# Optimization experiments

Measured on AMD Instinct MI355X. Metric: run time of the kernel, lower is better.

## Reference

```python
import jax, jax.numpy as jnp
import numpy as np

N_NODES = 50000
N_EDGES = 300000
N_ETYPES = 4
D = 256          # input_dim == output_dim (no zero-pad branch in GatedGraphConv)
RES = 768        # res_feature_dim
N_GRAPHS = 128
N_STEPS = 8
HID = 256        # classifier hidden dim


def setup_inputs() -> dict:
    key = jax.random.key(0)
    ks = jax.random.split(key, 12)
    s = 0.05
    return {
        "features": jax.random.normal(ks[0], (N_NODES, D + RES), jnp.float32),
        "W_e": jax.random.normal(ks[1], (N_ETYPES, D, D), jnp.float32) * s,
        "b_e": jnp.zeros((N_ETYPES, D), jnp.float32),
        "W_ih": jax.random.normal(ks[2], (D, 3 * D), jnp.float32) * s,
        "W_hh": jax.random.normal(ks[3], (D, 3 * D), jnp.float32) * s,
        "b_ih": jnp.zeros((3 * D,), jnp.float32),
        "b_hh": jnp.zeros((3 * D,), jnp.float32),
        "W1": jax.random.normal(ks[4], (D + RES, HID), jnp.float32) * s,
        "b1": jnp.zeros((HID,), jnp.float32),
        "W2": jax.random.normal(ks[5], (HID, 1), jnp.float32) * s,
        "b2": jnp.zeros((1,), jnp.float32),
        "src": jax.random.randint(ks[6], (N_EDGES,), 0, N_NODES),
        "dst": jax.random.randint(ks[7], (N_EDGES,), 0, N_NODES),
        "etypes": jax.random.randint(ks[8], (N_EDGES,), 0, N_ETYPES),
        "node2graph": jnp.sort(jax.random.randint(ks[9], (N_NODES,), 0, N_GRAPHS)),
    }


def _gru_cell(x, h, W_ih, W_hh, b_ih, b_hh):
    # PyTorch GRUCell, gate order (r, z, n)
    gi = x @ W_ih + b_ih
    gh = h @ W_hh + b_hh
    i_r, i_z, i_n = jnp.split(gi, 3, axis=-1)
    h_r, h_z, h_n = jnp.split(gh, 3, axis=-1)
    r = jax.nn.sigmoid(i_r + h_r)
    z = jax.nn.sigmoid(i_z + h_z)
    n = jnp.tanh(i_n + r * h_n)
    return (1.0 - z) * n + z * h


def reference(features, W_e, b_e, W_ih, W_hh, b_ih, b_hh, W1, b1, W2, b2,
              src, dst, etypes, node2graph):
    h = features[:, :D]          # node features fed to GGNN
    res = features[:, D:]        # mixed residual features (bypass GGNN)

    def step(h, _):
        # per-edge-type linear on all nodes: [T, N, D]
        ht = jnp.einsum('nd,tde->tne', h, W_e) + b_e[:, None, :]
        msgs = ht[etypes, src]                                   # [E, D]
        a = jax.ops.segment_sum(msgs, dst, num_segments=N_NODES)  # scatter-add to dst
        return _gru_cell(a, h, W_ih, W_hh, b_ih, b_hh), None

    h, _ = jax.lax.scan(step, h, None, length=N_STEPS)

    out = jnp.concatenate([h, res], axis=1)  # [N, D+RES]
    # masked mean over nodes of each graph == segment mean
    sums = jax.ops.segment_sum(out, node2graph, num_segments=N_GRAPHS)
    cnts = jax.ops.segment_sum(jnp.ones((N_NODES,), out.dtype), node2graph,
                               num_segments=N_GRAPHS)
    pooled = sums / jnp.maximum(cnts, 1.0)[:, None]  # [B, D+RES]

    # classifier (dropouts inactive at eval): Linear -> ReLU -> Linear -> sigmoid
    hcls = jax.nn.relu(pooled @ W1 + b1)
    logits = hcls @ W2 + b2
    return jax.nn.sigmoid(logits)  # [B, 1]
```

## Files before the change

### kernel.cpp

```cpp
#include <hip/hip_runtime.h>
#include <math.h>
#include <stdint.h>

#define NN 50000
#define NE 300000
#define NT4 200000
#define NG 128
#define NSTEP 8
#define MPAD 50048
#define SCB 196
#define SCB2 782
#define PCH 8
#define EM 64
#define ECAP 896

typedef __attribute__((ext_vector_type(8))) short bf16x8;
typedef __attribute__((ext_vector_type(8))) unsigned short u16x8;
typedef __attribute__((ext_vector_type(4))) float f32x4;
typedef unsigned short u16;
typedef unsigned int u32;

__device__ __forceinline__ float b2f(u16 u) {
  union { u32 i; float f; } c; c.i = ((u32)u) << 16; return c.f;
}
__device__ __forceinline__ u16 f2b(float f) {
  union { float f; u32 i; } c; c.f = f;
  u32 x = c.i;
  u32 r = (x + 0x7fffu + ((x >> 16) & 1u)) >> 16;
  return (u16)r;
}

__device__ __forceinline__ void load_lds16(const void* g, void* l) {
  __builtin_amdgcn_global_load_lds((const __attribute__((address_space(1))) u32*)g,
                                   (__attribute__((address_space(3))) u32*)l, 16, 0, 0);
}

__global__ void k_conv_we(const float* __restrict__ W_e, u16* __restrict__ Wt) {
  int i = blockIdx.x * 256 + threadIdx.x;
  int c = i >> 8, d = i & 255;
  Wt[c * 256 + d] = f2b(W_e[(c >> 8) * 65536 + d * 256 + (c & 255)]);
}
__global__ void k_conv_rz(const float* __restrict__ W_ih, const float* __restrict__ W_hh,
                          u16* __restrict__ ah, u16* __restrict__ ha) {
  int i = blockIdx.x * 256 + threadIdx.x;
  int n = i >> 9, k = i & 511;
  float va = (k < 256) ? W_ih[k * 768 + n] : W_hh[(k - 256) * 768 + n];
  float vh = (k < 256) ? W_hh[k * 768 + n] : W_ih[(k - 256) * 768 + n];
  ah[n * 512 + k] = f2b(va);
  ha[n * 512 + k] = f2b(vh);
}
__global__ void k_conv_n(const float* __restrict__ W, u16* __restrict__ Wt) {
  int i = blockIdx.x * 256 + threadIdx.x;
  int n = i >> 8, k = i & 255;
  Wt[n * 256 + k] = f2b(W[k * 768 + 512 + n]);
}
__global__ void k_brz(const float* __restrict__ b_ih, const float* __restrict__ b_hh,
                      float* __restrict__ b_rz) {
  int i = blockIdx.x * 256 + threadIdx.x;
  if (i < 512) b_rz[i] = b_ih[i] + b_hh[i];
}

__global__ void k_init_h(const float* __restrict__ feat, u16* __restrict__ acat) {
  int i = blockIdx.x * 256 + threadIdx.x;
  int n = i >> 6, d = (i & 63) << 2;
  ushort4 o;
  if (n < NN) {
    float4 v = *(const float4*)(feat + (size_t)n * 1024 + d);
    o.x = f2b(v.x); o.y = f2b(v.y); o.z = f2b(v.z); o.w = f2b(v.w);
  } else {
    o.x = o.y = o.z = o.w = 0;
  }
  *(ushort4*)(acat + (size_t)n * 768 + d) = o;
}

__global__ void k_hist(const int* __restrict__ dst, const int* __restrict__ ety,
                       int* __restrict__ deg2) {
  int e = blockIdx.x * 256 + threadIdx.x;
  if (e < NE) atomicAdd(&deg2[dst[e] * 4 + ety[e]], 1);
}
__global__ void k_scan1(const int* __restrict__ deg2, int* __restrict__ part, int* __restrict__ bsum) {
  __shared__ int sh[256];
  int b = blockIdx.x, t = threadIdx.x;
  int i = b * 256 + t;
  int v = (i < NT4) ? deg2[i] : 0;
  sh[t] = v;
  __syncthreads();
  for (int off = 1; off < 256; off <<= 1) {
    int tmp = (t >= off) ? sh[t - off] : 0;
    __syncthreads();
    sh[t] += tmp;
    __syncthreads();
  }
  if (i < NT4) part[i] = sh[t] - v;
  if (t == 255) bsum[b] = sh[255];
}
__global__ void k_scan2(const int* __restrict__ bsum, int* __restrict__ boff) {
  __shared__ int sh[1024];
  int t = threadIdx.x;
  int v = (t < SCB2) ? bsum[t] : 0;
  sh[t] = v;
  __syncthreads();
  for (int off = 1; off < 1024; off <<= 1) {
    int tmp = (t >= off) ? sh[t - off] : 0;
    __syncthreads();
    sh[t] += tmp;
    __syncthreads();
  }
  boff[t] = sh[t] - v;
  if (t == 1023) boff[1024] = sh[1023];
}
__global__ void k_scan3(const int* __restrict__ part, const int* __restrict__ boff, int* __restrict__ rp2) {
  int i = blockIdx.x * 256 + threadIdx.x;
  if (i < NT4) rp2[i] = part[i] + boff[i >> 8];
  if (i == NT4) rp2[NT4] = boff[1024];
}
__global__ void k_scatter(const int* __restrict__ src, const int* __restrict__ dst,
                          const int* __restrict__ ety, const int* __restrict__ rp2,
                          int* __restrict__ cursor2, int* __restrict__ esrc) {
  int e = blockIdx.x * 256 + threadIdx.x;
  if (e < NE) {
    int seg = dst[e] * 4 + ety[e];
    int p = rp2[seg] + atomicAdd(&cursor2[seg], 1);
    esrc[p] = src[e];
  }
}
__global__ void k_cnt2(const int* __restrict__ deg2, ushort4* __restrict__ cnt2) {
  int v = blockIdx.x * 256 + threadIdx.x;
  if (v >= MPAD) return;
  ushort4 o;
  if (v < NN) {
    o.x = (u16)deg2[v * 4 + 0]; o.y = (u16)deg2[v * 4 + 1];
    o.z = (u16)deg2[v * 4 + 2]; o.w = (u16)deg2[v * 4 + 3];
  } else {
    o.x = o.y = o.z = o.w = 0;
  }
  cnt2[v] = o;
}
__global__ void k_gstart(const int* __restrict__ n2g, int* __restrict__ gstart) {
  int n = blockIdx.x * 256 + threadIdx.x;
  if (n >= NN) return;
  int g = n2g[n];
  int gp = (n == 0) ? -1 : n2g[n - 1];
  for (int x = gp + 1; x <= g; ++x) gstart[x] = n;
  if (n == NN - 1)
    for (int x = g + 1; x <= NG; ++x) gstart[x] = NN;
}

__global__ __launch_bounds__(512, 4) void k_eagg(
    const u16* __restrict__ acat, int hboff,
    const int* __restrict__ rp2, const int* __restrict__ esrc,
    const u16* __restrict__ Wt_e, const u16* __restrict__ Wt_in,
    const ushort4* __restrict__ cnt2, const float* __restrict__ b_e,
    const float* __restrict__ b_ih512,
    u16* __restrict__ acat_out, u16* __restrict__ inb) {
  __shared__ __align__(16) char Ss[EM * 512];
  __shared__ __align__(16) char Bs[256 * 128];
  __shared__ int Es[ECAP];
  __shared__ int Rp[257];
  const int tid = threadIdx.x;
  const int wv = tid >> 6, l = tid & 63;
  const int hw = tid >> 5, lw = tid & 31;
  const int m0 = blockIdx.x * EM;
  const int fr = l & 15, kq = l >> 4;
  const int wm = (wv >> 2) * 32, wn = (wv & 3) * 64;

  const int base4 = m0 * 4;
  const int e0 = rp2[base4];
  for (int i = tid; i <= 256; i += 512) {
    int idx = base4 + i;
    if (idx > NT4) idx = NT4;
    Rp[i] = rp2[idx] - e0;
  }
  {
    int idxe = base4 + 256;
    if (idxe > NT4) idxe = NT4;
    int ecnt = rp2[idxe] - e0;
    int ecl = ecnt < ECAP ? ecnt : ECAP;
    for (int i = tid; i < ecl; i += 512) Es[i] = esrc[e0 + i] * 768 + hboff;
  }
  __syncthreads();

  f32x4 acc[2][4];
#pragma unroll
  for (int m = 0; m < 2; ++m)
#pragma unroll
    for (int n = 0; n < 4; ++n) acc[m][n] = (f32x4){0.f, 0.f, 0.f, 0.f};

  for (int t = 0; t < 4; ++t) {
    if (t > 0) __syncthreads();
    int cc[4], ee[4];
#pragma unroll
    for (int rr = 0; rr < 4; ++rr) {
      int li = (hw * 4 + rr) * 4 + t;
      cc[rr] = Rp[li];
      ee[rr] = Rp[li + 1];
    }
    float ar[4][8];
#pragma unroll
    for (int rr = 0; rr < 4; ++rr)
#pragma unroll
      for (int q = 0; q < 8; ++q) ar[rr][q] = 0.f;
    bool more = (cc[0] < ee[0]) | (cc[1] < ee[1]) | (cc[2] < ee[2]) | (cc[3] < ee[3]);
    while (more) {
      u16x8 v[4];
      bool p[4];
#pragma unroll
      for (int rr = 0; rr < 4; ++rr) {
        p[rr] = cc[rr] < ee[rr];
        if (p[rr]) {
          int rel = cc[rr];
          int off = (rel < ECAP) ? Es[rel] : (esrc[e0 + rel] * 768 + hboff);
          v[rr] = *(const u16x8*)(acat + (size_t)off + lw * 8);
        }
      }
#pragma unroll
      for (int rr = 0; rr < 4; ++rr) {
        if (p[rr]) {
#pragma unroll
          for (int q = 0; q < 8; ++q) ar[rr][q] += b2f(v[rr][q]);
          cc[rr]++;
        }
      }
      more = (cc[0] < ee[0]) | (cc[1] < ee[1]) | (cc[2] < ee[2]) | (cc[3] < ee[3]);
    }
#pragma unroll
    for (int rr = 0; rr < 4; ++rr) {
      int row = hw * 4 + rr;
      u16x8 o;
#pragma unroll
      for (int q = 0; q < 8; ++q) o[q] = f2b(ar[rr][q]);
      *(u16x8*)(Ss + row * 512 + ((lw * 16) ^ ((row & 7) << 4))) = o;
    }

    const u16* Bw = Wt_e + (size_t)t * 65536;
    for (int kc = 0; kc < 4; ++kc) {
      __syncthreads();
#pragma unroll
      for (int pph = 0; pph < 4; ++pph) {
        int brow = pph * 64 + (tid >> 3);
        int ks = kc * 64 + (((tid & 7) ^ (brow & 7)) << 3);
        load_lds16(Bw + (size_t)brow * 256 + ks, Bs + pph * 8192 + wv * 1024);
      }
      asm volatile("s_waitcnt vmcnt(0)" ::: "memory");
      __syncthreads();
#pragma unroll
      for (int kk = 0; kk < 64; kk += 32) {
        bf16x8 af[2], bfr[4];
        int kb = (kk + kq * 8) * 2;
        int ka = (kc * 64 + kk + kq * 8) * 2;
#pragma unroll
        for (int m = 0; m < 2; ++m) {
          int R = wm + m * 16 + fr;
          af[m] = *(const bf16x8*)(Ss + R * 512 + (ka ^ ((R & 7) << 4)));
        }
#pragma unroll
        for (int n = 0; n < 4; ++n) {
          int R = wn + n * 16 + fr;
          bfr[n] = *(const bf16x8*)(Bs + R * 128 + (kb ^ ((R & 7) << 4)));
        }
#pragma unroll
        for (int m = 0; m < 2; ++m)
#pragma unroll
          for (int n = 0; n < 4; ++n)
            acc[m][n] = __builtin_amdgcn_mfma_f32_16x16x32_bf16(af[m], bfr[n], acc[m][n], 0, 0, 0);
      }
    }
  }
  __syncthreads();

  float bev[4][4];
#pragma unroll
  for (int n = 0; n < 4; ++n)
#pragma unroll
    for (int t = 0; t < 4; ++t) bev[n][t] = b_e[t * 256 + wn + n * 16 + fr];
#pragma unroll
  for (int m = 0; m < 2; ++m) {
#pragma unroll
    for (int j = 0; j < 4; ++j) {
      int r = wm + m * 16 + kq * 4 + j;
      int v = m0 + r;
      ushort4 c4 = cnt2[v];
      float c0 = c4.x, c1 = c4.y, c2 = c4.z, c3 = c4.w;
#pragma unroll
      for (int n = 0; n < 4; ++n) {
        int col = wn + n * 16 + fr;
        float val = acc[m][n][j] + c0 * bev[n][0] + c1 * bev[n][1] + c2 * bev[n][2] + c3 * bev[n][3];
        u16 vb = f2b(val);
        acat_out[(size_t)v * 768 + 256 + col] = vb;
        *(u16*)(Ss + r * 512 + ((col * 2) ^ ((r & 7) << 4))) = vb;
      }
    }
  }
#pragma unroll
  for (int m = 0; m < 2; ++m)
#pragma unroll
    for (int n = 0; n < 4; ++n) acc[m][n] = (f32x4){0.f, 0.f, 0.f, 0.f};

  for (int kc = 0; kc < 4; ++kc) {
    __syncthreads();
#pragma unroll
    for (int pph = 0; pph < 4; ++pph) {
      int brow = pph * 64 + (tid >> 3);
      int ks = kc * 64 + (((tid & 7) ^ (brow & 7)) << 3);
      load_lds16(Wt_in + (size_t)brow * 256 + ks, Bs + pph * 8192 + wv * 1024);
    }
    asm volatile("s_waitcnt vmcnt(0)" ::: "memory");
    __syncthreads();
#pragma unroll
    for (int kk = 0; kk < 64; kk += 32) {
      bf16x8 af[2], bfr[4];
      int kb = (kk + kq * 8) * 2;
      int ka = (kc * 64 + kk + kq * 8) * 2;
#pragma unroll
      for (int m = 0; m < 2; ++m) {
        int R = wm + m * 16 + fr;
        af[m] = *(const bf16x8*)(Ss + R * 512 + (ka ^ ((R & 7) << 4)));
      }
#pragma unroll
      for (int n = 0; n < 4; ++n) {
        int R = wn + n * 16 + fr;
        bfr[n] = *(const bf16x8*)(Bs + R * 128 + (kb ^ ((R & 7) << 4)));
      }
#pragma unroll
      for (int m = 0; m < 2; ++m)
#pragma unroll
        for (int n = 0; n < 4; ++n)
          acc[m][n] = __builtin_amdgcn_mfma_f32_16x16x32_bf16(af[m], bfr[n], acc[m][n], 0, 0, 0);
    }
  }
  float bi[4];
#pragma unroll
  for (int n = 0; n < 4; ++n) bi[n] = b_ih512[wn + n * 16 + fr];
#pragma unroll
  for (int m = 0; m < 2; ++m) {
#pragma unroll
    for (int j = 0; j < 4; ++j) {
      int v = m0 + wm + m * 16 + kq * 4 + j;
#pragma unroll
      for (int n = 0; n < 4; ++n) {
        int col = wn + n * 16 + fr;
        inb[(size_t)v * 256 + col] = f2b(acc[m][n][j] + bi[n]);
      }
    }
  }
}

template <int MODE>
__global__ __launch_bounds__(512, 2) void k_gemm2(
    const u16* __restrict__ A, int lda, int K,
    const u16* __restrict__ Bt, const float* __restrict__ bias,
    u16* __restrict__ C, int ldc,
    const u16* __restrict__ rzb, const u16* __restrict__ inb,
    const u16* __restrict__ hold, u16* __restrict__ hnew) {
  __shared__ __align__(16) char AsB[2][64 * 128];
  __shared__ __align__(16) char BsB[2][256 * 128];
  const int tid = threadIdx.x;
  const int wv = tid >> 6, l = tid & 63;
  const int m0 = blockIdx.y * 64, n0 = blockIdx.x * 256;
  const int fr = l & 15, kq = l >> 4;
  const int wm = (wv >> 2) * 32, wn = (wv & 3) * 64;
  const int arow = tid >> 3, acl = tid & 7;

  f32x4 acc[2][4];
#pragma unroll
  for (int m = 0; m < 2; ++m)
#pragma unroll
    for (int n = 0; n < 4; ++n) acc[m][n] = (f32x4){0.f, 0.f, 0.f, 0.f};

  auto stage = [&](int buf, int k0) {
    load_lds16(A + (size_t)(m0 + arow) * lda + k0 + ((acl ^ (arow & 7)) << 3),
               AsB[buf] + wv * 1024);
#pragma unroll
    for (int p = 0; p < 4; ++p) {
      int brow = p * 64 + arow;
      load_lds16(Bt + (size_t)(n0 + brow) * K + k0 + ((acl ^ (brow & 7)) << 3),
                 BsB[buf] + p * 8192 + wv * 1024);
    }
  };

  stage(0, 0);
  const int NK = K >> 6;
  for (int ki = 0; ki < NK; ++ki) {
    const int cur = ki & 1;
    if (ki + 1 < NK) {
      stage(cur ^ 1, (ki + 1) << 6);
      asm volatile("s_waitcnt vmcnt(5)" ::: "memory");
    } else {
      asm volatile("s_waitcnt vmcnt(0)" ::: "memory");
    }
    __builtin_amdgcn_s_barrier();
    __builtin_amdgcn_sched_barrier(0);
    const char* As = AsB[cur];
    const char* Bs = BsB[cur];
#pragma unroll
    for (int kk = 0; kk < 64; kk += 32) {
      bf16x8 af[2], bfr[4];
      int kb = (kk + kq * 8) * 2;
#pragma unroll
      for (int m = 0; m < 2; ++m) {
        int R = wm + m * 16 + fr;
        af[m] = *(const bf16x8*)(As + R * 128 + (kb ^ ((R & 7) << 4)));
      }
#pragma unroll
      for (int n = 0; n < 4; ++n) {
        int R = wn + n * 16 + fr;
        bfr[n] = *(const bf16x8*)(Bs + R * 128 + (kb ^ ((R & 7) << 4)));
      }
#pragma unroll
      for (int m = 0; m < 2; ++m)
#pragma unroll
        for (int n = 0; n < 4; ++n)
          acc[m][n] = __builtin_amdgcn_mfma_f32_16x16x32_bf16(af[m], bfr[n], acc[m][n], 0, 0, 0);
    }
    asm volatile("s_waitcnt lgkmcnt(0)" ::: "memory");
    __builtin_amdgcn_sched_barrier(0);
    __builtin_amdgcn_s_barrier();
  }

#pragma unroll
  for (int m = 0; m < 2; ++m) {
#pragma unroll
    for (int j = 0; j < 4; ++j) {
      int row = m0 + wm + m * 16 + kq * 4 + j;
#pragma unroll
      for (int n = 0; n < 4; ++n) {
        int col = n0 + wn + n * 16 + fr;
        float v = acc[m][n][j] + bias[col];
        if (MODE == 1) {
          C[(size_t)row * ldc + col] = f2b(1.f / (1.f + expf(-v)));
        } else {
          float r = b2f(rzb[(size_t)row * 512 + col]);
          float z = b2f(rzb[(size_t)row * 512 + 256 + col]);
          float in_ = b2f(inb[(size_t)row * 256 + col]);
          float ho = b2f(hold[(size_t)row * 768 + col]);
          float ng = tanhf(in_ + r * v);
          hnew[(size_t)row * 768 + col] = f2b((1.f - z) * ng + z * ho);
        }
      }
    }
  }
}

__global__ __launch_bounds__(256) void k_pool(const u16* __restrict__ hb, const float* __restrict__ feat,
                                              const int* __restrict__ gstart, float* __restrict__ pooled) {
  int g = blockIdx.x, ch = blockIdx.y, t = threadIdx.x;
  int s = gstart[g], e = gstart[g + 1];
  int tot = e - s;
  int per = (tot + PCH - 1) / PCH;
  int ns = s + ch * per;
  int ne = ns + per < e ? ns + per : e;
  if (ns >= ne) return;
  int c = t << 2;
  float a0 = 0.f, a1 = 0.f, a2 = 0.f, a3 = 0.f;
  if (c < 256) {
    for (int n = ns; n < ne; ++n) {
      ushort4 u = *(const ushort4*)(hb + (size_t)n * 768 + c);
      a0 += b2f(u.x); a1 += b2f(u.y); a2 += b2f(u.z); a3 += b2f(u.w);
    }
  } else {
    for (int n = ns; n < ne; ++n) {
      float4 v = *(const float4*)(feat + (size_t)n * 1024 + c);
      a0 += v.x; a1 += v.y; a2 += v.z; a3 += v.w;
    }
  }
  atomicAdd(&pooled[g * 1024 + c], a0);
  atomicAdd(&pooled[g * 1024 + c + 1], a1);
  atomicAdd(&pooled[g * 1024 + c + 2], a2);
  atomicAdd(&pooled[g * 1024 + c + 3], a3);
}

__global__ __launch_bounds__(256) void k_head(const float* __restrict__ pooled,
                                              const int* __restrict__ gstart,
                                              const float* __restrict__ W1, const float* __restrict__ b1,
                                              const float* __restrict__ W2, const float* __restrict__ b2,
                                              float* __restrict__ out) {
  __shared__ float sp[1024];
  __shared__ float red[256];
  int g = blockIdx.x, t = threadIdx.x;
  float inv = 1.f / fmaxf((float)(gstart[g + 1] - gstart[g]), 1.f);
  for (int i = t; i < 1024; i += 256) sp[i] = pooled[g * 1024 + i] * inv;
  __syncthreads();
  float acc = b1[t];
  for (int k = 0; k < 1024; ++k) acc += sp[k] * W1[k * 256 + t];
  float hc = fmaxf(acc, 0.f);
  red[t] = hc * W2[t];
  __syncthreads();
  for (int s2 = 128; s2 > 0; s2 >>= 1) {
    if (t < s2) red[t] += red[t + s2];
    __syncthreads();
  }
  if (t == 0) out[g] = 1.f / (1.f + expf(-(red[0] + b2[0])));
}

extern "C" void kernel_launch(void* const* d_in, const int* in_sizes, int n_in, void* d_out, int out_size,
                              void* d_ws, size_t ws_size, hipStream_t stream) {
  const float* feat = (const float*)d_in[0];
  const float* W_e = (const float*)d_in[1];
  const float* b_e = (const float*)d_in[2];
  const float* W_ih = (const float*)d_in[3];
  const float* W_hh = (const float*)d_in[4];
  const float* b_ih = (const float*)d_in[5];
  const float* b_hh = (const float*)d_in[6];
  const float* W1 = (const float*)d_in[7];
  const float* b1 = (const float*)d_in[8];
  const float* W2 = (const float*)d_in[9];
  const float* b2 = (const float*)d_in[10];
  const int* src = (const int*)d_in[11];
  const int* dst = (const int*)d_in[12];
  const int* ety = (const int*)d_in[13];
  const int* n2g = (const int*)d_in[14];

  char* p = (char*)d_ws;
  auto alloc = [&](size_t b) { char* r = p; p += (b + 255) & ~(size_t)255; return r; };
  u16* acat = (u16*)alloc((size_t)MPAD * 768 * 2);
  u16* rzb = (u16*)alloc((size_t)MPAD * 512 * 2);
  u16* inb = (u16*)alloc((size_t)MPAD * 256 * 2);
  u16* Wt_e = (u16*)alloc(1024 * 256 * 2);
  u16* Wt_rz_ah = (u16*)alloc(512 * 512 * 2);
  u16* Wt_rz_ha = (u16*)alloc(512 * 512 * 2);
  u16* Wt_in = (u16*)alloc(256 * 256 * 2);
  u16* Wt_hn = (u16*)alloc(256 * 256 * 2);
  float* b_rz = (float*)alloc(512 * 4);
  int* deg2 = (int*)alloc((size_t)NT4 * 4);
  int* part = (int*)alloc((size_t)NT4 * 4);
  int* bsum = (int*)alloc((size_t)SCB2 * 4);
  int* boff = (int*)alloc(1025 * 4);
  int* rp2 = (int*)alloc((size_t)(NT4 + 1) * 4);
  int* cursor2 = (int*)alloc((size_t)NT4 * 4);
  int* esrc = (int*)alloc((size_t)NE * 4);
  ushort4* cnt2 = (ushort4*)alloc((size_t)MPAD * 8);
  int* gstart = (int*)alloc((size_t)(NG + 1) * 4);
  float* pooled = (float*)alloc((size_t)NG * 1024 * 4);

  hipMemsetAsync(deg2, 0, (size_t)NT4 * 4, stream);
  hipMemsetAsync(cursor2, 0, (size_t)NT4 * 4, stream);
  hipMemsetAsync(pooled, 0, (size_t)NG * 1024 * 4, stream);

  k_conv_we<<<1024, 256, 0, stream>>>(W_e, Wt_e);
  k_conv_rz<<<1024, 256, 0, stream>>>(W_ih, W_hh, Wt_rz_ah, Wt_rz_ha);
  k_conv_n<<<256, 256, 0, stream>>>(W_ih, Wt_in);
  k_conv_n<<<256, 256, 0, stream>>>(W_hh, Wt_hn);
  k_brz<<<2, 256, 0, stream>>>(b_ih, b_hh, b_rz);
  k_init_h<<<MPAD / 4, 256, 0, stream>>>(feat, acat);
  k_hist<<<(NE + 255) / 256, 256, 0, stream>>>(dst, ety, deg2);
  k_scan1<<<SCB2, 256, 0, stream>>>(deg2, part, bsum);
  k_scan2<<<1, 1024, 0, stream>>>(bsum, boff);
  k_scan3<<<SCB2 + 1, 256, 0, stream>>>(part, boff, rp2);
  k_scatter<<<(NE + 255) / 256, 256, 0, stream>>>(src, dst, ety, rp2, cursor2, esrc);
  k_cnt2<<<(MPAD + 255) / 256, 256, 0, stream>>>(deg2, cnt2);
  k_gstart<<<SCB, 256, 0, stream>>>(n2g, gstart);

  const int GY = MPAD / 64;
  for (int s = 0; s < NSTEP; ++s) {
    int hboff = (s & 1) ? 512 : 0;
    int hnewoff = 512 - hboff;
    int rzoff = (s & 1) ? 256 : 0;
    const u16* Wrz = (s & 1) ? Wt_rz_ah : Wt_rz_ha;
    k_eagg<<<MPAD / EM, 512, 0, stream>>>(acat, hboff, rp2, esrc, Wt_e, Wt_in, cnt2, b_e,
                                          b_ih + 512, acat, inb);
    k_gemm2<1><<<dim3(2, GY), 512, 0, stream>>>(acat + rzoff, 768, 512, Wrz, b_rz, rzb, 512,
                                                nullptr, nullptr, nullptr, nullptr);
    k_gemm2<2><<<dim3(1, GY), 512, 0, stream>>>(acat + hboff, 768, 256, Wt_hn, b_hh + 512,
                                                nullptr, 0, rzb, inb, acat + hboff,
                                                acat + hnewoff);
  }

  k_pool<<<dim3(NG, PCH), 256, 0, stream>>>(acat, feat, gstart, pooled);
  k_head<<<NG, 256, 0, stream>>>(pooled, gstart, W1, b1, W2, b2, (float*)d_out);
}
```

Measured before the change: 1.678 ms.

## Double-buffer weight tiles in k_eagg with prefetch across edge-type and input GEMMs

Replaces the single 32KB weight staging buffer with two 16KB buffers holding 32-wide K chunks. A unified chunk index spans all four edge-type weight slices and the W_in slice, so the next chunk's async global-to-LDS load is issued while MFMAs run on the current one. This hides load latency that was previously serialized behind s_waitcnt vmcnt(0) and the barriers, and it also prefetches the first chunk during the gather phase. The cost is a new LDS swizzle layout and hand-placed waitcnt/barrier and sched_barrier calls, which are fragile to get right.

```diff
diff --git a/kernel.cpp b/kernel.cpp
--- a/kernel.cpp
+++ b/kernel.cpp
@@ -154,7 +154,7 @@
     const float* __restrict__ b_ih512,
     u16* __restrict__ acat_out, u16* __restrict__ inb) {
   __shared__ __align__(16) char Ss[EM * 512];
-  __shared__ __align__(16) char Bs[256 * 128];
+  __shared__ __align__(16) char BsB[2][16384];
   __shared__ int Es[ECAP];
   __shared__ int Rp[257];
   const int tid = threadIdx.x;
@@ -178,7 +178,21 @@
     int ecl = ecnt < ECAP ? ecnt : ECAP;
     for (int i = tid; i < ecl; i += 512) Es[i] = esrc[e0 + i] * 768 + hboff;
   }
+
+  auto stageB = [&](int buf, int c) {
+    const u16* W = (c < 32) ? (Wt_e + ((size_t)(c >> 3) << 16)) : Wt_in;
+    int kbase = (c & 7) << 5;
+#pragma unroll
+    for (int p = 0; p < 2; ++p) {
+      int i = p * 512 + tid;
+      int row = i >> 2, slot = i & 3;
+      load_lds16(W + (size_t)row * 256 + kbase + ((slot ^ ((row >> 1) & 3)) << 3),
+                 BsB[buf] + p * 8192 + wv * 1024);
+    }
+  };
+
   __syncthreads();
+  stageB(0, 0);
 
   f32x4 acc[2][4];
 #pragma unroll
@@ -187,7 +201,6 @@
     for (int n = 0; n < 4; ++n) acc[m][n] = (f32x4){0.f, 0.f, 0.f, 0.f};
 
   for (int t = 0; t < 4; ++t) {
-    if (t > 0) __syncthreads();
     int cc[4], ee[4];
 #pragma unroll
     for (int rr = 0; rr < 4; ++rr) {
@@ -231,42 +244,39 @@
       for (int q = 0; q < 8; ++q) o[q] = f2b(ar[rr][q]);
       *(u16x8*)(Ss + row * 512 + ((lw * 16) ^ ((row & 7) << 4))) = o;
     }
-
-    const u16* Bw = Wt_e + (size_t)t * 65536;
-    for (int kc = 0; kc < 4; ++kc) {
-      __syncthreads();
-#pragma unroll
-      for (int pph = 0; pph < 4; ++pph) {
-        int brow = pph * 64 + (tid >> 3);
-        int ks = kc * 64 + (((tid & 7) ^ (brow & 7)) << 3);
-        load_lds16(Bw + (size_t)brow * 256 + ks, Bs + pph * 8192 + wv * 1024);
-      }
-      asm volatile("s_waitcnt vmcnt(0)" ::: "memory");
-      __syncthreads();
-#pragma unroll
-      for (int kk = 0; kk < 64; kk += 32) {
-        bf16x8 af[2], bfr[4];
-        int kb = (kk + kq * 8) * 2;
-        int ka = (kc * 64 + kk + kq * 8) * 2;
-#pragma unroll
-        for (int m = 0; m < 2; ++m) {
-          int R = wm + m * 16 + fr;
-          af[m] = *(const bf16x8*)(Ss + R * 512 + (ka ^ ((R & 7) << 4)));
-        }
-#pragma unroll
-        for (int n = 0; n < 4; ++n) {
-          int R = wn + n * 16 + fr;
-          bfr[n] = *(const bf16x8*)(Bs + R * 128 + (kb ^ ((R & 7) << 4)));
-        }
-#pragma unroll
-        for (int m = 0; m < 2; ++m)
-#pragma unroll
-          for (int n = 0; n < 4; ++n)
-            acc[m][n] = __builtin_amdgcn_mfma_f32_16x16x32_bf16(af[m], bfr[n], acc[m][n], 0, 0, 0);
-      }
-    }
-  }
-  __syncthreads();
+    asm volatile("s_waitcnt lgkmcnt(0)" ::: "memory");
+    __builtin_amdgcn_sched_barrier(0);
+
+    for (int kc = 0; kc < 8; ++kc) {
+      const int c = t * 8 + kc;
+      const int buf = c & 1;
+      stageB(buf ^ 1, c + 1);
+      asm volatile("s_waitcnt vmcnt(2)" ::: "memory");
+      __builtin_amdgcn_s_barrier();
+      __builtin_amdgcn_sched_barrier(0);
+      const char* BsC = BsB[buf];
+      const int ka2 = (kc << 6) + (kq << 4);
+      bf16x8 af[2], bfr[4];
+#pragma unroll
+      for (int m = 0; m < 2; ++m) {
+        int R = wm + m * 16 + fr;
+        af[m] = *(const bf16x8*)(Ss + R * 512 + (ka2 ^ ((R & 7) << 4)));
+      }
+#pragma unroll
+      for (int n = 0; n < 4; ++n) {
+        int R = wn + n * 16 + fr;
+        bfr[n] = *(const bf16x8*)(BsC + R * 64 + ((kq ^ ((R >> 1) & 3)) << 4));
+      }
+#pragma unroll
+      for (int m = 0; m < 2; ++m)
+#pragma unroll
+        for (int n = 0; n < 4; ++n)
+          acc[m][n] = __builtin_amdgcn_mfma_f32_16x16x32_bf16(af[m], bfr[n], acc[m][n], 0, 0, 0);
+      asm volatile("s_waitcnt lgkmcnt(0)" ::: "memory");
+      __builtin_amdgcn_sched_barrier(0);
+      __builtin_amdgcn_s_barrier();
+    }
+  }
 
   float bev[4][4];
 #pragma unroll
@@ -295,39 +305,43 @@
   for (int m = 0; m < 2; ++m)
 #pragma unroll
     for (int n = 0; n < 4; ++n) acc[m][n] = (f32x4){0.f, 0.f, 0.f, 0.f};
-
-  for (int kc = 0; kc < 4; ++kc) {
-    __syncthreads();
-#pragma unroll
-    for (int pph = 0; pph < 4; ++pph) {
-      int brow = pph * 64 + (tid >> 3);
-      int ks = kc * 64 + (((tid & 7) ^ (brow & 7)) << 3);
-      load_lds16(Wt_in + (size_t)brow * 256 + ks, Bs + pph * 8192 + wv * 1024);
-    }
-    asm volatile("s_waitcnt vmcnt(0)" ::: "memory");
-    __syncthreads();
-#pragma unroll
-    for (int kk = 0; kk < 64; kk += 32) {
-      bf16x8 af[2], bfr[4];
-      int kb = (kk + kq * 8) * 2;
-      int ka = (kc * 64 + kk + kq * 8) * 2;
-#pragma unroll
-      for (int m = 0; m < 2; ++m) {
-        int R = wm + m * 16 + fr;
-        af[m] = *(const bf16x8*)(Ss + R * 512 + (ka ^ ((R & 7) << 4)));
-      }
-#pragma unroll
-      for (int n = 0; n < 4; ++n) {
-        int R = wn + n * 16 + fr;
-        bfr[n] = *(const bf16x8*)(Bs + R * 128 + (kb ^ ((R & 7) << 4)));
-      }
-#pragma unroll
-      for (int m = 0; m < 2; ++m)
-#pragma unroll
-        for (int n = 0; n < 4; ++n)
-          acc[m][n] = __builtin_amdgcn_mfma_f32_16x16x32_bf16(af[m], bfr[n], acc[m][n], 0, 0, 0);
-    }
-  }
+  asm volatile("s_waitcnt lgkmcnt(0)" ::: "memory");
+  __builtin_amdgcn_sched_barrier(0);
+
+  for (int kc = 0; kc < 8; ++kc) {
+    const int c = 32 + kc;
+    const int buf = c & 1;
+    if (kc < 7) {
+      stageB(buf ^ 1, c + 1);
+      asm volatile("s_waitcnt vmcnt(2)" ::: "memory");
+    } else {
+      asm volatile("s_waitcnt vmcnt(0)" ::: "memory");
+    }
+    __builtin_amdgcn_s_barrier();
+    __builtin_amdgcn_sched_barrier(0);
+    const char* BsC = BsB[buf];
+    const int ka2 = (kc << 6) + (kq << 4);
+    bf16x8 af[2], bfr[4];
+#pragma unroll
+    for (int m = 0; m < 2; ++m) {
+      int R = wm + m * 16 + fr;
+      af[m] = *(const bf16x8*)(Ss + R * 512 + (ka2 ^ ((R & 7) << 4)));
+    }
+#pragma unroll
+    for (int n = 0; n < 4; ++n) {
+      int R = wn + n * 16 + fr;
+      bfr[n] = *(const bf16x8*)(BsC + R * 64 + ((kq ^ ((R >> 1) & 3)) << 4));
+    }
+#pragma unroll
+    for (int m = 0; m < 2; ++m)
+#pragma unroll
+      for (int n = 0; n < 4; ++n)
+        acc[m][n] = __builtin_amdgcn_mfma_f32_16x16x32_bf16(af[m], bfr[n], acc[m][n], 0, 0, 0);
+    asm volatile("s_waitcnt lgkmcnt(0)" ::: "memory");
+    __builtin_amdgcn_sched_barrier(0);
+    __builtin_amdgcn_s_barrier();
+  }
+
   float bi[4];
 #pragma unroll
   for (int n = 0; n < 4; ++n) bi[n] = b_ih512[wn + n * 16 + fr];
```

Result: no change. 1.673 ms (-0.3%).
